# Kernel tuning notes

Hardware: AMD Instinct MI355X
Metric: run time of the kernel (lower is better)

The kernel has to match this reference:

```python
import jax, jax.numpy as jnp
import numpy as np

DIM = 256
H = 4
K = 16
R = 4
EPS = 1e-5


def _conv1x1(x, W, b):
    # x: [B, Cin, N, P], W: [Cout, Cin], b: [Cout]
    return jnp.einsum('oc,bcnp->bonp', W, x) + b[None, :, None, None]


def setup_inputs() -> dict:
    key = jax.random.key(0)
    ks = jax.random.split(key, 12)
    B, N = 4, 8192
    s = 1.0 / np.sqrt(DIM)
    inp = {
        'queries': jax.random.normal(ks[0], (B, DIM, N, R), dtype=jnp.float32),
        'feats': jax.random.normal(ks[1], (B, DIM, N, K), dtype=jnp.float32),
        'Wq': jax.random.normal(ks[2], (DIM, DIM), dtype=jnp.float32) * s,
        'bq': jnp.zeros((DIM,), dtype=jnp.float32),
        'Wk': jax.random.normal(ks[3], (DIM, DIM), dtype=jnp.float32) * s,
        'bk': jnp.zeros((DIM,), dtype=jnp.float32),
        'Wv': jax.random.normal(ks[4], (DIM, DIM), dtype=jnp.float32) * s,
        'bv': jnp.zeros((DIM,), dtype=jnp.float32),
        'W1': jax.random.normal(ks[5], (2 * DIM, DIM), dtype=jnp.float32) * s,
        'b1': jnp.zeros((2 * DIM,), dtype=jnp.float32),
        'gamma': jnp.ones((2 * DIM,), dtype=jnp.float32),
        'beta': jnp.zeros((2 * DIM,), dtype=jnp.float32),
        'W2': jax.random.normal(ks[6], (DIM, 2 * DIM), dtype=jnp.float32) * (1.0 / np.sqrt(2 * DIM)),
        'b2': jnp.zeros((DIM,), dtype=jnp.float32),
    }
    return inp


def reference(queries, feats, Wq, bq, Wk, bk, Wv, bv, W1, b1, gamma, beta, W2, b2):
    B, _, N, _ = feats.shape
    d = DIM // H
    queries_iden = queries  # [B, dim, N, r]

    q = _conv1x1(queries, Wq, bq).reshape(B, H, d, N, R)   # [B,h,d,N,r]
    k = _conv1x1(feats, Wk, bk).reshape(B, H, d, N, K)     # [B,h,d,N,K]
    v = _conv1x1(feats, Wv, bv).reshape(B, H, d, N, K)     # [B,h,d,N,K]

    # logits: [B,N,h,r,K]
    logits = jnp.einsum('bhdnr,bhdnk->bnhrk', q, k) * (d ** -0.5)
    soft = jax.nn.softmax(logits, axis=-1)
    # agg: [B,N,h,r,d] -> permute to [B,N,h,d,r] -> [B,N,dim,r] -> [B,dim,N,r]
    agg = jnp.einsum('bnhrk,bhdnk->bnhdr', soft, v)
    agg = agg.reshape(B, N, DIM, R).transpose(0, 2, 1, 3)
    agg = agg + queries_iden

    # FFN: conv1x1 -> BN (training-mode batch stats) -> ReLU -> conv1x1, residual, ReLU
    h1 = _conv1x1(agg, W1, b1)  # [B, 2*dim, N, r]
    mean = jnp.mean(h1, axis=(0, 2, 3), keepdims=True)
    var = jnp.var(h1, axis=(0, 2, 3), keepdims=True)
    h1 = (h1 - mean) * jax.lax.rsqrt(var + EPS)
    h1 = h1 * gamma[None, :, None, None] + beta[None, :, None, None]
    h1 = jax.nn.relu(h1)
    h2 = _conv1x1(h1, W2, b2)
    return jax.nn.relu(h2 + agg)
```

## Files before the change

kernel.cpp:

```cpp
#include <hip/hip_runtime.h>
#include <hip/hip_bf16.h>

#define NB 4
#define NRQ 32768
#define NKF 131072

using u16 = unsigned short;
typedef short bf16x8 __attribute__((ext_vector_type(8)));
typedef float f32x4  __attribute__((ext_vector_type(4)));
typedef u16   u16x8  __attribute__((ext_vector_type(8)));
typedef u16   u16x4  __attribute__((ext_vector_type(4)));
typedef u16   u16x2  __attribute__((ext_vector_type(2)));

#if defined(__has_builtin)
#  if __has_builtin(__builtin_amdgcn_fdot2_f32_bf16)
#    define HAVE_DOT2 1
#  endif
#endif
#ifndef HAVE_DOT2
#  define HAVE_DOT2 0
#endif

#if HAVE_DOT2
typedef __bf16 bfv2 __attribute__((ext_vector_type(2)));
union bpack { bf16x8 v; bfv2 p[4]; };
__device__ __forceinline__ float dot2(bfv2 a, bfv2 b, float c){
  return __builtin_amdgcn_fdot2_f32_bf16(a, b, c, false);
}
#endif
union vpack { bf16x8 v; u16 e[8]; };

__device__ __forceinline__ u16 f2b(float f){
  __hip_bfloat16 h = __float2bfloat16(f);
  return *reinterpret_cast<u16*>(&h);
}
__device__ __forceinline__ float b2f(u16 v){
  return __uint_as_float(((unsigned)v) << 16);
}

#define GLOAD16(g, l) __builtin_amdgcn_global_load_lds( \
    (const __attribute__((address_space(1))) unsigned int*)(g), \
    (__attribute__((address_space(3))) unsigned int*)(l), 16, 0, 0)

__global__ __launch_bounds__(256) void cvtW_k(
    const float* __restrict__ Wk, const float* __restrict__ Wv,
    const float* __restrict__ Wq, const float* __restrict__ W1,
    const float* __restrict__ W2, u16* __restrict__ wT,
    const float* __restrict__ bk, const float* __restrict__ bv,
    float* __restrict__ bKV, float* __restrict__ stats)
{
  if (blockIdx.x >= 224){
    int i = (blockIdx.x - 224) * 256 + threadIdx.x;
    if (i < 512)       bKV[i] = (i < 256) ? bk[i] : bv[i - 256];
    else if (i < 1536) stats[i - 512] = 0.f;
    return;
  }
  long e = ((long)blockIdx.x * 256 + threadIdx.x) * 8;
  const float* src; long off;
  if      (e < 65536)  { src = Wk; off = e; }
  else if (e < 131072) { src = Wv; off = e - 65536; }
  else if (e < 196608) { src = Wq; off = e - 131072; }
  else if (e < 327680) { src = W1; off = e - 196608; }
  else                 { src = W2; off = e - 327680; }
  float4 f0 = *reinterpret_cast<const float4*>(src + off);
  float4 f1 = *reinterpret_cast<const float4*>(src + off + 4);
  u16x8 p;
  p[0]=f2b(f0.x); p[1]=f2b(f0.y); p[2]=f2b(f0.z); p[3]=f2b(f0.w);
  p[4]=f2b(f1.x); p[5]=f2b(f1.y); p[6]=f2b(f1.z); p[7]=f2b(f1.w);
  *reinterpret_cast<u16x8*>(wT + e) = p;
}

__global__ __launch_bounds__(256) void transpose_k(
    const float* __restrict__ in, u16* __restrict__ out,
    int NCtot, long outBatch)
{
  __shared__ u16 sT[64][264];
  const int t = threadIdx.x, b = blockIdx.y;
  const int nr0 = blockIdx.x * 64;
  const int cb = t >> 2, nrq = t & 3;
  const long ib = (long)b * 256 * NCtot + nr0;

  #pragma unroll
  for (int ci = 0; ci < 4; ++ci){
    const int c = cb + ci * 64;
    const float* src = in + ib + (long)c * NCtot + nrq * 16;
    #pragma unroll
    for (int j = 0; j < 4; ++j){
      float4 f = *reinterpret_cast<const float4*>(src + j * 4);
      int nr = nrq * 16 + j * 4;
      sT[nr+0][c] = f2b(f.x); sT[nr+1][c] = f2b(f.y);
      sT[nr+2][c] = f2b(f.z); sT[nr+3][c] = f2b(f.w);
    }
  }
  __syncthreads();
  const int row = t >> 2, qtr = t & 3;
  u16* orow = out + (long)b * outBatch + (long)(nr0 + row) * 256 + qtr * 64;
  #pragma unroll
  for (int i = 0; i < 8; ++i)
    *reinterpret_cast<u16x8*>(orow + i * 8) =
        *reinterpret_cast<const u16x8*>(&sT[row][qtr * 64 + i * 8]);
}

template<int MODE, int KD>
__global__ __launch_bounds__(256) void gemm_k(
    const u16* __restrict__ A, long aBatch, int chTiles,
    const u16* __restrict__ Wb, const float* __restrict__ bias,
    u16* __restrict__ outH, long oBatch, int NCH,
    float* __restrict__ statSum, float* __restrict__ statSq,
    const float* __restrict__ xsc, const float* __restrict__ xsh,
    const u16* __restrict__ residT,
    float* __restrict__ outF, long fBatch)
{
  __shared__ __align__(16) char sA[2][16384];
  __shared__ __align__(16) char sB[2][16384];

  const int t = threadIdx.x, lane = t & 63, wid = t >> 6;
  const int wm = wid >> 1, wn = wid & 1;
  const int b = blockIdx.z;

  const int nwg = gridDim.x, orig = blockIdx.x;
  const int qq = nwg >> 3, rr = nwg & 7, xcd = orig & 7, pos = orig >> 3;
  const int wg = (xcd < rr ? xcd * (qq + 1) : rr * (qq + 1) + (xcd - rr) * qq) + pos;
  const int rowT = wg / chTiles, chT = wg % chTiles;

  const u16* Ab = A + (long)b * aBatch + (long)rowT * 128 * KD;
  const u16* Wt = Wb + (long)chT * 128 * KD;
  const int sub = lane >> 3, kc8 = ((lane & 7) ^ sub) * 8;

  f32x4 acc[4][4];
  #pragma unroll
  for (int i = 0; i < 4; ++i)
    #pragma unroll
    for (int j = 0; j < 4; ++j) acc[i][j] = (f32x4){0.f,0.f,0.f,0.f};

  auto STAGE = [&](int buf, int ks){
    const int k0 = ks * 64;
    if constexpr (MODE == 3){
      const int wrow = t >> 1, whalf = t & 1;
      const u16* arow = Ab + (long)wrow * KD + k0 + whalf * 32;
      #pragma unroll
      for (int i = 0; i < 4; ++i){
        u16x8 v = *reinterpret_cast<const u16x8*>(arow + i * 8);
        const int kb = k0 + whalf*32 + i*8;
        float4 s0 = *reinterpret_cast<const float4*>(xsc + kb);
        float4 s1 = *reinterpret_cast<const float4*>(xsc + kb + 4);
        float4 h0 = *reinterpret_cast<const float4*>(xsh + kb);
        float4 h1 = *reinterpret_cast<const float4*>(xsh + kb + 4);
        u16x8 o;
        o[0]=f2b(fmaxf(b2f(v[0])*s0.x+h0.x,0.f));
        o[1]=f2b(fmaxf(b2f(v[1])*s0.y+h0.y,0.f));
        o[2]=f2b(fmaxf(b2f(v[2])*s0.z+h0.z,0.f));
        o[3]=f2b(fmaxf(b2f(v[3])*s0.w+h0.w,0.f));
        o[4]=f2b(fmaxf(b2f(v[4])*s1.x+h1.x,0.f));
        o[5]=f2b(fmaxf(b2f(v[5])*s1.y+h1.y,0.f));
        o[6]=f2b(fmaxf(b2f(v[6])*s1.z+h1.z,0.f));
        o[7]=f2b(fmaxf(b2f(v[7])*s1.w+h1.w,0.f));
        *reinterpret_cast<u16x8*>(
            sA[buf] + ((wrow*128 + whalf*64 + i*16) ^ ((wrow & 7) << 4))) = o;
      }
      #pragma unroll
      for (int i = 0; i < 4; ++i){
        const int chunk = wid * 4 + i;
        GLOAD16(Wt + (long)(chunk*8 + sub)*KD + k0 + kc8, sB[buf] + chunk*1024);
      }
    } else {
      #pragma unroll
      for (int i = 0; i < 4; ++i){
        const int chunk = wid * 4 + i;
        GLOAD16(Ab + (long)(chunk*8 + sub)*KD + k0 + kc8, sA[buf] + chunk*1024);
        GLOAD16(Wt + (long)(chunk*8 + sub)*KD + k0 + kc8, sB[buf] + chunk*1024);
      }
    }
  };

  constexpr int NT = KD / 64;
  STAGE(0, 0);
  __syncthreads();
  int cur = 0;
  for (int ks = 0; ks < NT; ++ks){
    if (ks + 1 < NT) STAGE(cur ^ 1, ks + 1);
    const char* pA = sA[cur]; const char* pB = sB[cur];
    #pragma unroll
    for (int kk = 0; kk < 2; ++kk){
      bf16x8 af[4], bf[4];
      #pragma unroll
      for (int mi = 0; mi < 4; ++mi){
        int m = wm*64 + mi*16 + (lane & 15);
        af[mi] = *reinterpret_cast<const bf16x8*>(
            pA + ((m*128 + kk*64 + (lane>>4)*16) ^ ((m & 7) << 4)));
      }
      #pragma unroll
      for (int ni = 0; ni < 4; ++ni){
        int c = wn*64 + ni*16 + (lane & 15);
        bf[ni] = *reinterpret_cast<const bf16x8*>(
            pB + ((c*128 + kk*64 + (lane>>4)*16) ^ ((c & 7) << 4)));
      }
      #pragma unroll
      for (int mi = 0; mi < 4; ++mi)
        #pragma unroll
        for (int ni = 0; ni < 4; ++ni)
          acc[mi][ni] = __builtin_amdgcn_mfma_f32_16x16x32_bf16(
              af[mi], bf[ni], acc[mi][ni], 0, 0, 0);
    }
    __syncthreads();
    cur ^= 1;
  }

  int chI[4]; float bv[4];
  #pragma unroll
  for (int ni = 0; ni < 4; ++ni){
    int ch = chT*128 + wn*64 + ni*16 + (lane & 15);
    chI[ni] = ch;
    bv[ni] = bias[ch];
  }
  if (MODE != 3){
    float s[4] = {0,0,0,0}, sq[4] = {0,0,0,0};
    u16* outb = outH + (long)b * oBatch;
    #pragma unroll
    for (int mi = 0; mi < 4; ++mi){
      #pragma unroll
      for (int j = 0; j < 4; ++j){
        const long row = rowT*128 + wm*64 + mi*16 + (lane>>4)*4 + j;
        #pragma unroll
        for (int ni = 0; ni < 4; ++ni){
          float v = acc[mi][ni][j] + bv[ni];
          outb[row * NCH + chI[ni]] = f2b(v);
          if (MODE == 1){ s[ni] += v; sq[ni] += v * v; }
        }
      }
    }
    if (MODE == 1){
      #pragma unroll
      for (int ni = 0; ni < 4; ++ni){
        s[ni]  += __shfl_xor(s[ni], 16);  s[ni]  += __shfl_xor(s[ni], 32);
        sq[ni] += __shfl_xor(sq[ni], 16); sq[ni] += __shfl_xor(sq[ni], 32);
      }
      if (lane < 16){
        #pragma unroll
        for (int ni = 0; ni < 4; ++ni){
          atomicAdd(&statSum[chI[ni]], s[ni]);
          atomicAdd(&statSq[chI[ni]],  sq[ni]);
        }
      }
    }
  } else {
    const u16* rb = residT + (long)b * ((long)NRQ * 256);
    #pragma unroll
    for (int mi = 0; mi < 4; ++mi){
      const int nr0 = rowT*128 + wm*64 + mi*16 + (lane>>4)*4;
      #pragma unroll
      for (int ni = 0; ni < 4; ++ni){
        float4 o;
        o.x = fmaxf(acc[mi][ni][0] + bv[ni] + b2f(rb[(long)(nr0+0)*256 + chI[ni]]), 0.f);
        o.y = fmaxf(acc[mi][ni][1] + bv[ni] + b2f(rb[(long)(nr0+1)*256 + chI[ni]]), 0.f);
        o.z = fmaxf(acc[mi][ni][2] + bv[ni] + b2f(rb[(long)(nr0+2)*256 + chI[ni]]), 0.f);
        o.w = fmaxf(acc[mi][ni][3] + bv[ni] + b2f(rb[(long)(nr0+3)*256 + chI[ni]]), 0.f);
        *reinterpret_cast<float4*>(outF + (long)b*fBatch + (long)chI[ni]*NRQ + nr0) = o;
      }
    }
  }
}

__global__ __launch_bounds__(512, 4) void kvattn_k(
    const float* __restrict__ feats, const u16* __restrict__ wKV,
    const float* __restrict__ bKV, const u16* __restrict__ qT,
    const u16* __restrict__ qrT, u16* __restrict__ aggT)
{
  __shared__ __align__(16) char LDS[74752];
  char*  sAg = LDS;
  char*  sW  = LDS + 9216;
  char*  sK  = LDS;
  char*  sV  = LDS + 33792;
  float* sSf = (float*)(LDS + 67072);

  const int t = threadIdx.x, lane = t & 63, wid = t >> 6;
  const int wr = wid >> 2, wc = wid & 3;
  const int b = blockIdx.y;
  const long row0 = (long)blockIdx.x * 64;

  const int chL = t >> 4, nq = t & 15;
  const float* fbase = feats + (long)b * 256 * NKF + row0 + nq * 4;

  auto STAGEW = [&](int buf, int ks){
    const int k0 = ks * 32;
    #pragma unroll
    for (int i = 0; i < 4; ++i){
      const int cw = wid * 4 + i;
      const int ch = cw * 16 + (lane >> 2), jd = lane & 3;
      GLOAD16(wKV + (long)ch * 256 + k0 + ((jd ^ ((ch >> 1) & 3)) * 8),
              sW + buf * 32768 + cw * 1024);
    }
  };
  auto WRITEA = [&](int buf, float4 f){
    #pragma unroll
    for (int i = 0; i < 4; ++i){
      const int r = nq * 4 + i;
      float e = (i == 0) ? f.x : (i == 1) ? f.y : (i == 2) ? f.z : f.w;
      *reinterpret_cast<u16*>(sAg + buf*4608 + r*72 + chL*2) = f2b(e);
    }
  };

  f32x4 acc[2][8];
  #pragma unroll
  for (int i = 0; i < 2; ++i)
    #pragma unroll
    for (int j = 0; j < 8; ++j) acc[i][j] = (f32x4){0.f,0.f,0.f,0.f};

  float4 aReg0, aReg1;
  {
    aReg0 = *reinterpret_cast<const float4*>(fbase + (long)chL * NKF);
    aReg1 = *reinterpret_cast<const float4*>(fbase + (long)(32 + chL) * NKF);
    STAGEW(0, 0);
    WRITEA(0, aReg0);
  }
  __syncthreads();

  int cur = 0;
  const int jq = lane >> 4;
  #pragma unroll
  for (int ks = 0; ks < 8; ++ks){
    if (ks < 7) STAGEW(cur ^ 1, ks + 1);
    __builtin_amdgcn_sched_barrier(0);
    if (ks < 6){
      float4 f = *reinterpret_cast<const float4*>(
          fbase + (long)((ks + 2) * 32 + chL) * NKF);
      if ((ks & 1) == 0) aReg0 = f; else aReg1 = f;
    }
    const char* pA = sAg + cur * 4608;
    const char* pW = sW  + cur * 32768;
    bf16x8 af[2];
    #pragma unroll
    for (int mi = 0; mi < 2; ++mi){
      const int m = wr*32 + mi*16 + (lane & 15);
      af[mi] = *reinterpret_cast<const bf16x8*>(pA + m*72 + jq*16);
    }
    __builtin_amdgcn_s_setprio(1);
    #pragma unroll
    for (int ni = 0; ni < 8; ++ni){
      const int ch = wc*128 + ni*16 + (lane & 15);
      bf16x8 bf = *reinterpret_cast<const bf16x8*>(
          pW + ch*64 + (((jq ^ ((ch>>1)&3)) * 16)));
      acc[0][ni] = __builtin_amdgcn_mfma_f32_16x16x32_bf16(af[0], bf, acc[0][ni], 0,0,0);
      acc[1][ni] = __builtin_amdgcn_mfma_f32_16x16x32_bf16(af[1], bf, acc[1][ni], 0,0,0);
    }
    __builtin_amdgcn_s_setprio(0);
    if (ks < 7) WRITEA(cur ^ 1, ((ks + 1) & 1) == 0 ? aReg0 : aReg1);
    if (ks < 6){
      asm volatile("s_waitcnt vmcnt(1) lgkmcnt(0)" ::: "memory");
    } else {
      asm volatile("s_waitcnt vmcnt(0) lgkmcnt(0)" ::: "memory");
    }
    __builtin_amdgcn_s_barrier();
    cur ^= 1;
  }

  {
    float bv[8];
    #pragma unroll
    for (int ni = 0; ni < 8; ++ni) bv[ni] = bKV[wc*128 + ni*16 + (lane & 15)];
    if (wc < 2){
      #pragma unroll
      for (int mi = 0; mi < 2; ++mi){
        const int p2 = wr*2 + mi;
        #pragma unroll
        for (int ni = 0; ni < 8; ++ni){
          const int ch = wc*128 + ni*16 + (lane & 15);
          #pragma unroll
          for (int j = 0; j < 4; ++j){
            const int kk2 = (lane>>4)*4 + j;
            *reinterpret_cast<u16*>(
                sK + (p2*16 + kk2)*528 + ((ch*2) ^ ((kk2 & 7) << 4))) =
                f2b(acc[mi][ni][j] + bv[ni]);
          }
        }
      }
    } else {
      #pragma unroll
      for (int mi = 0; mi < 2; ++mi){
        const int p2 = wr*2 + mi;
        #pragma unroll
        for (int ni = 0; ni < 8; ++ni){
          const int cv = (wc-2)*128 + ni*16 + (lane & 15);
          #pragma unroll
          for (int j = 0; j < 4; ++j){
            const int kk2 = (lane>>4)*4 + j;
            *reinterpret_cast<u16*>(sV + (p2*16 + kk2)*520 + cv*2) =
                f2b(acc[mi][ni][j] + bv[ni]);
          }
        }
      }
    }
  }

  const int p = wid & 3, rh = wid >> 2;
  const int nqg = blockIdx.x * 4 + p;
  const int c0 = rh*128 + lane*2;
  u16x2 rq[4];
  {
    const u16* rqp = qrT + ((long)b*NRQ + (long)nqg*4)*256 + c0;
    #pragma unroll
    for (int r = 0; r < 4; ++r)
      rq[r] = *reinterpret_cast<const u16x2*>(rqp + r*256);
  }
  __syncthreads();

  {
    const int h = lane >> 4, kk = lane & 15;
    const u16* qb = qT + ((long)b*NRQ + (long)nqg*4 + rh*2)*256 + h*64;
    const char* kr = sK + (p*16 + kk)*528;
    float l0 = 0.f, l1 = 0.f;
#if HAVE_DOT2
    #pragma unroll
    for (int d8 = 0; d8 < 8; ++d8){
      bpack K8, Q0, Q1;
      K8.v = *reinterpret_cast<const bf16x8*>(
          kr + ((h*128 + d8*16) ^ ((kk & 7) << 4)));
      Q0.v = *reinterpret_cast<const bf16x8*>(qb + d8*8);
      Q1.v = *reinterpret_cast<const bf16x8*>(qb + 256 + d8*8);
      #pragma unroll
      for (int pi = 0; pi < 4; ++pi){
        l0 = dot2(K8.p[pi], Q0.p[pi], l0);
        l1 = dot2(K8.p[pi], Q1.p[pi], l1);
      }
    }
#else
    #pragma unroll
    for (int d8 = 0; d8 < 8; ++d8){
      vpack K8, Q0, Q1;
      K8.v = *reinterpret_cast<const bf16x8*>(
          kr + ((h*128 + d8*16) ^ ((kk & 7) << 4)));
      Q0.v = *reinterpret_cast<const bf16x8*>(qb + d8*8);
      Q1.v = *reinterpret_cast<const bf16x8*>(qb + 256 + d8*8);
      #pragma unroll
      for (int e = 0; e < 8; ++e){
        float kf = b2f(K8.e[e]);
        l0 = fmaf(kf, b2f(Q0.e[e]), l0);
        l1 = fmaf(kf, b2f(Q1.e[e]), l1);
      }
    }
#endif
    float pr[2]; float lv[2] = {l0, l1};
    #pragma unroll
    for (int r = 0; r < 2; ++r){
      float x = lv[r] * 0.125f;
      float m = x;
      #pragma unroll
      for (int off = 1; off < 16; off <<= 1) m = fmaxf(m, __shfl_xor(m, off));
      float e = __expf(x - m);
      float ssum = e;
      #pragma unroll
      for (int off = 1; off < 16; off <<= 1) ssum += __shfl_xor(ssum, off);
      pr[r] = e / ssum;
    }
    *reinterpret_cast<float2*>(sSf + (p*4 + (lane>>4))*68 + (lane&15)*4 + rh*2) =
        make_float2(pr[0], pr[1]);
  }
  __syncthreads();

  {
    const int h = c0 >> 6;
    const char* vrow = sV + (p*16)*520;
    const float* ss = sSf + (p*4 + h)*68;
    float a[4][2] = {};
    #pragma unroll
    for (int kk = 0; kk < 16; ++kk){
      u16x2 vv = *reinterpret_cast<const u16x2*>(vrow + kk*520 + c0*2);
      float4 sv = *reinterpret_cast<const float4*>(ss + kk*4);
      float v0 = b2f(vv[0]), v1 = b2f(vv[1]);
      a[0][0] += sv.x*v0; a[0][1] += sv.x*v1;
      a[1][0] += sv.y*v0; a[1][1] += sv.y*v1;
      a[2][0] += sv.z*v0; a[2][1] += sv.z*v1;
      a[3][0] += sv.w*v0; a[3][1] += sv.w*v1;
    }
    u16* ob = aggT + ((long)b*NRQ + (long)nqg*4)*256 + c0;
    #pragma unroll
    for (int r = 0; r < 4; ++r){
      u16x2 pk;
      pk[0] = f2b(a[r][0] + b2f(rq[r][0]));
      pk[1] = f2b(a[r][1] + b2f(rq[r][1]));
      *reinterpret_cast<u16x2*>(ob + r*256) = pk;
    }
  }
}

__global__ void finalize_k(const float* __restrict__ st,
                           const float* __restrict__ gamma,
                           const float* __restrict__ beta,
                           float* __restrict__ out)
{
  int o = blockIdx.x*256 + threadIdx.x;
  const float inv = 1.f / 131072.f;
  float mean = st[o] * inv;
  float var  = st[512 + o] * inv - mean*mean;
  float sc   = gamma[o] * rsqrtf(var + 1e-5f);
  out[o]       = sc;
  out[512 + o] = beta[o] - mean * sc;
}

extern "C" void kernel_launch(void* const* d_in, const int* in_sizes, int n_in,
                              void* d_out, int out_size, void* d_ws, size_t ws_size,
                              hipStream_t stream)
{
  (void)in_sizes; (void)n_in; (void)out_size; (void)ws_size;
  const float* queries = (const float*)d_in[0];
  const float* feats   = (const float*)d_in[1];
  const float* Wq = (const float*)d_in[2];
  const float* bq = (const float*)d_in[3];
  const float* Wk = (const float*)d_in[4];
  const float* bk = (const float*)d_in[5];
  const float* Wv = (const float*)d_in[6];
  const float* bv = (const float*)d_in[7];
  const float* W1 = (const float*)d_in[8];
  const float* b1 = (const float*)d_in[9];
  const float* gamma = (const float*)d_in[10];
  const float* beta  = (const float*)d_in[11];
  const float* W2 = (const float*)d_in[12];
  const float* b2 = (const float*)d_in[13];

  char* ws = (char*)d_ws;
  u16*   h1T   = (u16*)ws;
  u16*   qrT   = (u16*)(ws + 134217728L);
  u16*   qT    = (u16*)(ws + 201326592L);
  u16*   aggT  = (u16*)(ws + 268435456L);
  float* stats = (float*)(ws + 335544320L);
  float* scale = stats + 1024;
  float* shift = stats + 1536;
  u16*   wT    = (u16*)(ws + 335552512L);
  u16*   wKV   = wT;
  u16*   wQ    = wT + 131072;
  u16*   wW1   = wT + 196608;
  u16*   wW2   = wT + 327680;
  float* bKV   = (float*)(wT + 458752);

  cvtW_k<<<dim3(230), 256, 0, stream>>>(Wk, Wv, Wq, W1, W2, wT,
                                        bk, bv, bKV, stats);

  transpose_k<<<dim3(NRQ/64, NB), 256, 0, stream>>>(queries, qrT, NRQ, (long)NRQ*256);

  gemm_k<0, 256><<<dim3(512, 1, NB), 256, 0, stream>>>(
      qrT, (long)NRQ*256, 2, wQ, bq,
      qT, (long)NRQ*256, 256, nullptr, nullptr, nullptr, nullptr,
      nullptr, nullptr, 0);

  kvattn_k<<<dim3(NKF/64, NB), 512, 0, stream>>>(
      feats, wKV, bKV, qT, qrT, aggT);

  gemm_k<1, 256><<<dim3(1024, 1, NB), 256, 0, stream>>>(
      aggT, (long)NRQ*256, 4, wW1, b1,
      h1T, (long)NRQ*512, 512, stats, stats + 512, nullptr, nullptr,
      nullptr, nullptr, 0);

  finalize_k<<<dim3(2), 256, 0, stream>>>(stats, gamma, beta, scale);

  gemm_k<3, 512><<<dim3(512, 1, NB), 256, 0, stream>>>(
      h1T, (long)NRQ*512, 2, wW2, b2,
      nullptr, 0, 256, nullptr, nullptr, scale, shift,
      aggT, (float*)d_out, (long)256*NRQ);
}
```

Before: 663.1 us.

## Simplify feats staging to scalar strided loads and drop K-tile XOR swizzle

Replaces the float4 feats loads, which were prefetched two steps ahead, with four scalar loads per thread strided by 16 rows and fetched one step ahead. The hand-tuned s_waitcnt/s_barrier sequence becomes a plain __syncthreads. The XOR swizzle on the K tile in LDS is removed, and the K and V epilogue writes are merged into one code path. This trades prefetch depth and wide loads for simpler code and possibly fewer LDS write conflicts in the staging layout, but it risks exposing global load latency and adding LDS bank conflicts on the unswizzled K reads.

```diff
diff --git a/kernel.cpp b/kernel.cpp
--- a/kernel.cpp
+++ b/kernel.cpp
@@ -23,12 +23,12 @@
 
 #if HAVE_DOT2
 typedef __bf16 bfv2 __attribute__((ext_vector_type(2)));
-union bpack { bf16x8 v; bfv2 p[4]; };
+union bpack  { bf16x8 v; bfv2 p[4]; };
 __device__ __forceinline__ float dot2(bfv2 a, bfv2 b, float c){
   return __builtin_amdgcn_fdot2_f32_bf16(a, b, c, false);
 }
 #endif
-union vpack { bf16x8 v; u16 e[8]; };
+union vpack  { bf16x8 v; u16 e[8]; };
 
 __device__ __forceinline__ u16 f2b(float f){
   __hip_bfloat16 h = __float2bfloat16(f);
@@ -279,7 +279,7 @@
   const long row0 = (long)blockIdx.x * 64;
 
   const int chL = t >> 4, nq = t & 15;
-  const float* fbase = feats + (long)b * 256 * NKF + row0 + nq * 4;
+  const float* fbase = feats + (long)b * 256 * NKF + row0 + nq;
 
   auto STAGEW = [&](int buf, int ks){
     const int k0 = ks * 32;
@@ -291,12 +291,16 @@
               sW + buf * 32768 + cw * 1024);
     }
   };
-  auto WRITEA = [&](int buf, float4 f){
+  auto LOADA = [&](int ks, float* ar){
+    const float* src = fbase + (long)(ks * 32 + chL) * NKF;
+    #pragma unroll
+    for (int i = 0; i < 4; ++i) ar[i] = src[16 * i];
+  };
+  auto WRITEA = [&](int buf, const float* ar){
     #pragma unroll
     for (int i = 0; i < 4; ++i){
-      const int r = nq * 4 + i;
-      float e = (i == 0) ? f.x : (i == 1) ? f.y : (i == 2) ? f.z : f.w;
-      *reinterpret_cast<u16*>(sAg + buf*4608 + r*72 + chL*2) = f2b(e);
+      const int r = nq + 16 * i;
+      *reinterpret_cast<u16*>(sAg + buf*4608 + r*72 + chL*2) = f2b(ar[i]);
     }
   };
 
@@ -306,12 +310,11 @@
     #pragma unroll
     for (int j = 0; j < 8; ++j) acc[i][j] = (f32x4){0.f,0.f,0.f,0.f};
 
-  float4 aReg0, aReg1;
+  float aR[4];
   {
-    aReg0 = *reinterpret_cast<const float4*>(fbase + (long)chL * NKF);
-    aReg1 = *reinterpret_cast<const float4*>(fbase + (long)(32 + chL) * NKF);
+    LOADA(0, aR);
     STAGEW(0, 0);
-    WRITEA(0, aReg0);
+    WRITEA(0, aR);
   }
   __syncthreads();
 
@@ -319,12 +322,9 @@
   const int jq = lane >> 4;
   #pragma unroll
   for (int ks = 0; ks < 8; ++ks){
-    if (ks < 7) STAGEW(cur ^ 1, ks + 1);
-    __builtin_amdgcn_sched_barrier(0);
-    if (ks < 6){
-      float4 f = *reinterpret_cast<const float4*>(
-          fbase + (long)((ks + 2) * 32 + chL) * NKF);
-      if ((ks & 1) == 0) aReg0 = f; else aReg1 = f;
+    if (ks < 7){
+      LOADA(ks + 1, aR);
+      STAGEW(cur ^ 1, ks + 1);
     }
     const char* pA = sAg + cur * 4608;
     const char* pW = sW  + cur * 32768;
@@ -344,13 +344,8 @@
       acc[1][ni] = __builtin_amdgcn_mfma_f32_16x16x32_bf16(af[1], bf, acc[1][ni], 0,0,0);
     }
     __builtin_amdgcn_s_setprio(0);
-    if (ks < 7) WRITEA(cur ^ 1, ((ks + 1) & 1) == 0 ? aReg0 : aReg1);
-    if (ks < 6){
-      asm volatile("s_waitcnt vmcnt(1) lgkmcnt(0)" ::: "memory");
-    } else {
-      asm volatile("s_waitcnt vmcnt(0) lgkmcnt(0)" ::: "memory");
-    }
-    __builtin_amdgcn_s_barrier();
+    if (ks < 7) WRITEA(cur ^ 1, aR);
+    __syncthreads();
     cur ^= 1;
   }
 
@@ -358,35 +353,19 @@
     float bv[8];
     #pragma unroll
     for (int ni = 0; ni < 8; ++ni) bv[ni] = bKV[wc*128 + ni*16 + (lane & 15)];
-    if (wc < 2){
-      #pragma unroll
-      for (int mi = 0; mi < 2; ++mi){
-        const int p2 = wr*2 + mi;
+    char* dst = (wc < 2) ? sK : sV;
+    const int pitch = (wc < 2) ? 528 : 520;
+    const int chb = (wc & 1) * 128;
+    #pragma unroll
+    for (int mi = 0; mi < 2; ++mi){
+      #pragma unroll
+      for (int ni = 0; ni < 8; ++ni){
+        const int ch = chb + ni*16 + (lane & 15);
         #pragma unroll
-        for (int ni = 0; ni < 8; ++ni){
-          const int ch = wc*128 + ni*16 + (lane & 15);
-          #pragma unroll
-          for (int j = 0; j < 4; ++j){
-            const int kk2 = (lane>>4)*4 + j;
-            *reinterpret_cast<u16*>(
-                sK + (p2*16 + kk2)*528 + ((ch*2) ^ ((kk2 & 7) << 4))) =
-                f2b(acc[mi][ni][j] + bv[ni]);
-          }
-        }
-      }
-    } else {
-      #pragma unroll
-      for (int mi = 0; mi < 2; ++mi){
-        const int p2 = wr*2 + mi;
-        #pragma unroll
-        for (int ni = 0; ni < 8; ++ni){
-          const int cv = (wc-2)*128 + ni*16 + (lane & 15);
-          #pragma unroll
-          for (int j = 0; j < 4; ++j){
-            const int kk2 = (lane>>4)*4 + j;
-            *reinterpret_cast<u16*>(sV + (p2*16 + kk2)*520 + cv*2) =
-                f2b(acc[mi][ni][j] + bv[ni]);
-          }
+        for (int j = 0; j < 4; ++j){
+          const int r = wr*32 + mi*16 + (lane>>4)*4 + j;
+          *reinterpret_cast<u16*>(dst + r*pitch + ch*2) =
+              f2b(acc[mi][ni][j] + bv[ni]);
         }
       }
     }
@@ -407,14 +386,13 @@
   {
     const int h = lane >> 4, kk = lane & 15;
     const u16* qb = qT + ((long)b*NRQ + (long)nqg*4 + rh*2)*256 + h*64;
-    const char* kr = sK + (p*16 + kk)*528;
+    const char* kr = sK + (p*16 + kk)*528 + h*128;
     float l0 = 0.f, l1 = 0.f;
 #if HAVE_DOT2
     #pragma unroll
     for (int d8 = 0; d8 < 8; ++d8){
       bpack K8, Q0, Q1;
-      K8.v = *reinterpret_cast<const bf16x8*>(
-          kr + ((h*128 + d8*16) ^ ((kk & 7) << 4)));
+      K8.v = *reinterpret_cast<const bf16x8*>(kr + d8*16);
       Q0.v = *reinterpret_cast<const bf16x8*>(qb + d8*8);
       Q1.v = *reinterpret_cast<const bf16x8*>(qb + 256 + d8*8);
       #pragma unroll
@@ -427,8 +405,7 @@
     #pragma unroll
     for (int d8 = 0; d8 < 8; ++d8){
       vpack K8, Q0, Q1;
-      K8.v = *reinterpret_cast<const bf16x8*>(
-          kr + ((h*128 + d8*16) ^ ((kk & 7) << 4)));
+      K8.v = *reinterpret_cast<const bf16x8*>(kr + d8*16);
       Q0.v = *reinterpret_cast<const bf16x8*>(qb + d8*8);
       Q1.v = *reinterpret_cast<const bf16x8*>(qb + 256 + d8*8);
       #pragma unroll
@@ -452,7 +429,7 @@
       for (int off = 1; off < 16; off <<= 1) ssum += __shfl_xor(ssum, off);
       pr[r] = e / ssum;
     }
-    *reinterpret_cast<float2*>(sSf + (p*4 + (lane>>4))*68 + (lane&15)*4 + rh*2) =
+    *reinterpret_cast<float2*>(sSf + (p*4 + h)*68 + kk*4 + rh*2) =
         make_float2(pr[0], pr[1]);
   }
   __syncthreads();
```

New measurement: 679.8 us. 1.03x slower.
